# Optimization experiments

Measured on AMD Instinct MI355X. Metric: run time of the kernel, lower is better.

Reference implementation:

```python
import jax, jax.numpy as jnp
import numpy as np

EPS = 0.05      # entropic regularization, matches eps arg in forward
ITERS = 100     # Sinkhorn fixed-point iterations (auction analog; converged math)

def setup_inputs() -> dict:
    key = jax.random.key(0)
    k1, k2 = jax.random.split(key)
    B, N, D = 16, 2048, 3
    x = jax.random.uniform(k1, (B, N, D), dtype=jnp.float32)
    y = jax.random.uniform(k2, (B, N, D), dtype=jnp.float32)
    return {"x": x, "y": y}

def _emd_mean(x, y):
    # pairwise squared distances: [B, N, N]
    x2 = jnp.sum(x * x, axis=-1)                      # [B, N]
    y2 = jnp.sum(y * y, axis=-1)                      # [B, N]
    xy = jnp.einsum('bnd,bmd->bnm', x, y)             # [B, N, N]
    C = x2[:, :, None] + y2[:, None, :] - 2.0 * xy
    C = jnp.maximum(C, 0.0)

    B, N, _ = C.shape
    logK = -C / EPS                                   # [B, N, N]
    log_mu = jnp.full((B, N), -jnp.log(jnp.float32(N)))
    log_nu = log_mu

    def body(carry, _):
        f, g = carry
        # f_i = eps*(log mu_i - logsumexp_j((g_j - C_ij)/eps))
        f = EPS * (log_mu - jax.nn.logsumexp(logK + (g / EPS)[:, None, :], axis=2))
        g = EPS * (log_nu - jax.nn.logsumexp(logK + (f / EPS)[:, :, None], axis=1))
        return (f, g), None

    f0 = jnp.zeros((B, N), dtype=C.dtype)
    g0 = jnp.zeros((B, N), dtype=C.dtype)
    (f, g), _ = jax.lax.scan(body, (f0, g0), None, length=ITERS)

    # transport plan P_ij = exp((f_i + g_j - C_ij)/eps) (already includes mu,nu)
    logP = (f[:, :, None] + g[:, None, :] - C) / EPS
    P = jnp.exp(logP)
    # per-source-point matched squared distance, scaled by N (row mass = 1/N)
    dis = jnp.sum(P * C, axis=2) * N                  # [B, N]
    return dis.mean()

def reference(x, y):
    return _emd_mean(x, y)
```

## Files before the change

### kernel.cpp

```cpp
#include <hip/hip_runtime.h>

#define BB 16
#define NN 2048
#define NITERS 100

#define K2E      28.853900817779268f
#define TWO_K2E  57.707801635558536f
#define INV2K    0.017328679513998632f
#define INV_K2E  0.034657359027997264f
#define INV4K    0.008664339756999316f
#define LMU      (-11.0f)

#if __has_builtin(__builtin_amdgcn_exp2f)
#define EXP2F(x) __builtin_amdgcn_exp2f(x)
#else
#define EXP2F(x) exp2f(x)
#endif

typedef float v2f __attribute__((ext_vector_type(2)));
typedef float v4f __attribute__((ext_vector_type(4)));

#define DSTORE(p, v) __hip_atomic_store((p), (v), __ATOMIC_RELAXED, __HIP_MEMORY_SCOPE_AGENT)
#define DLOAD(p)     __hip_atomic_load((p), __ATOMIC_RELAXED, __HIP_MEMORY_SCOPE_AGENT)

__device__ __forceinline__ float bfly8(const float acc[8], int lane) {
    const bool b0 = lane & 1, b1 = lane & 2, b2 = lane & 4;
    float v4[4], v2_[2], v1;
    #pragma unroll
    for (int i = 0; i < 4; ++i) {
        float recv = __shfl_xor(b0 ? acc[i] : acc[i+4], 1, 64);
        v4[i] = (b0 ? acc[i+4] : acc[i]) + recv;
    }
    #pragma unroll
    for (int i = 0; i < 2; ++i) {
        float recv = __shfl_xor(b1 ? v4[i] : v4[i+2], 2, 64);
        v2_[i] = (b1 ? v4[i+2] : v4[i]) + recv;
    }
    {
        float recv = __shfl_xor(b2 ? v2_[0] : v2_[1], 4, 64);
        v1 = (b2 ? v2_[1] : v2_[0]) + recv;
    }
    v1 += __shfl_xor(v1, 8, 64);
    v1 += __shfl_xor(v1, 16, 64);
    v1 += __shfl_xor(v1, 32, 64);
    return v1;
}

__device__ __forceinline__ float sumpassF(
    const v4f* __restrict__ U, const v4f* __restrict__ T,
    const float* __restrict__ sdv,
    int rloc, int lane)
{
    v2f xp0[4], xp1[4], xp2[4], acc2[4];
    #pragma unroll
    for (int p = 0; p < 4; ++p) {
        const v4f ua = U[rloc + 2*p];
        const v4f ub = U[rloc + 2*p + 1];
        xp0[p] = (v2f){ua.x * INV2K, ub.x * INV2K};
        xp1[p] = (v2f){ua.y * INV2K, ub.y * INV2K};
        xp2[p] = (v2f){ua.z * INV2K, ub.z * INV2K};
        acc2[p] = (v2f){0.f, 0.f};
    }
    #pragma unroll 4
    for (int s = 0; s < 32; ++s) {
        const int p = lane + (s << 6);
        const v4f t = T[p];
        const float ad = sdv[p];
        const v2f a0v = (v2f){t.x, t.x}, a1v = (v2f){t.y, t.y};
        const v2f a2v = (v2f){t.z, t.z}, adv = (v2f){ad, ad};
        #pragma unroll
        for (int qq = 0; qq < 4; ++qq) {
            v2f d = __builtin_elementwise_fma(xp0[qq], a0v,
                    __builtin_elementwise_fma(xp1[qq], a1v,
                    __builtin_elementwise_fma(xp2[qq], a2v, adv)));
            acc2[qq] += (v2f){EXP2F(d.x), EXP2F(d.y)};
        }
    }
    float acc[8];
    #pragma unroll
    for (int p = 0; p < 4; ++p) { acc[2*p] = acc2[p].x; acc[2*p+1] = acc2[p].y; }
    return bfly8(acc, lane);
}

__device__ __forceinline__ float sumpassL(
    const v4f* __restrict__ U, const v4f* __restrict__ T,
    const float* __restrict__ sdv,
    int rloc, int jh, int lane, int w, float* pcomb)
{
    const int jb = (jh << 10) + lane;
    float dv[16];
    #pragma unroll
    for (int s = 0; s < 16; ++s)
        dv[s] = sdv[jb + (s << 6)];

    v2f xp0[4], xp1[4], xp2[4], acc2[4];
    #pragma unroll
    for (int p = 0; p < 4; ++p) {
        const v4f ua = U[rloc + 2*p];
        const v4f ub = U[rloc + 2*p + 1];
        xp0[p] = (v2f){ua.x * INV2K, ub.x * INV2K};
        xp1[p] = (v2f){ua.y * INV2K, ub.y * INV2K};
        xp2[p] = (v2f){ua.z * INV2K, ub.z * INV2K};
        acc2[p] = (v2f){0.f, 0.f};
    }
    #pragma unroll 4
    for (int s = 0; s < 16; ++s) {
        const v4f t = T[jb + (s << 6)];
        const float ad = dv[s];
        const v2f a0v = (v2f){t.x, t.x}, a1v = (v2f){t.y, t.y};
        const v2f a2v = (v2f){t.z, t.z}, adv = (v2f){ad, ad};
        #pragma unroll
        for (int qq = 0; qq < 4; ++qq) {
            v2f d = __builtin_elementwise_fma(xp0[qq], a0v,
                    __builtin_elementwise_fma(xp1[qq], a1v,
                    __builtin_elementwise_fma(xp2[qq], a2v, adv)));
            acc2[qq] += (v2f){EXP2F(d.x), EXP2F(d.y)};
        }
    }
    float acc[8];
    #pragma unroll
    for (int p = 0; p < 4; ++p) { acc[2*p] = acc2[p].x; acc[2*p+1] = acc2[p].y; }
    float v1 = bfly8(acc, lane);
    const int rr = ((lane & 1) << 2) | (lane & 2) | ((lane >> 2) & 1);
    if (lane < 8) pcomb[w * 8 + rr] = v1;
    __syncthreads();
    float Sc = 0.f;
    if (lane < 8) Sc = v1 + pcomb[(w ^ 1) * 8 + rr];
    return Sc;
}

__device__ __forceinline__ float epilA(
    const v4f* __restrict__ U, const v4f* __restrict__ T,
    const float* __restrict__ gB,
    float Aval, int rloc, int jh, int lane)
{
    const int jb = (jh << 10) + lane;
    float dv[16];
    #pragma unroll
    for (int s = 0; s < 16; ++s)
        dv[s] = DLOAD(gB + jb + (s << 6));

    float xr0[8], xr1[8], xr2[8], Ak[8], x2k[8];
    #pragma unroll
    for (int k = 0; k < 8; ++k) {
        const v4f u = U[rloc + k];
        xr0[k] = u.x * INV2K;
        xr1[k] = u.y * INV2K;
        xr2[k] = u.z * INV2K;
        const int src = ((k & 1) << 2) | (k & 2) | ((k >> 2) & 1);
        Ak[k]  = __shfl(Aval, src, 64);
        x2k[k] = K2E * (xr0[k]*xr0[k] + xr1[k]*xr1[k] + xr2[k]*xr2[k]);
    }
    float acc = 0.f;
    for (int s = 0; s < 16; ++s) {
        const v4f t = T[jb + (s << 6)];
        const float a0 = t.x, a1 = t.y, a2 = t.z, tb = dv[s];
        const float q2 = (a0*a0 + a1*a1 + a2*a2) * INV4K;
        #pragma unroll
        for (int k = 0; k < 8; ++k) {
            float d = fmaf(xr0[k], a0, fmaf(xr1[k], a1, fmaf(xr2[k], a2, tb)));
            float P = EXP2F(d + Ak[k]);
            float C = fmaxf((x2k[k] + q2 - (d - tb)) * INV_K2E, 0.f);
            acc = fmaf(P, C, acc);
        }
    }
    return acc;
}

__global__ __launch_bounds__(1024, 4) void emd_sinkhornU(
    const float* __restrict__ x, const float* __restrict__ y,
    float* __restrict__ Af, float* __restrict__ Bf,
    int* __restrict__ flags, float* __restrict__ out)
{
    extern __shared__ float S[];
    __shared__ float wsum[16];

    const int tid  = threadIdx.x;
    const int lane = tid & 63;
    const int w    = tid >> 6;
    const int blk  = blockIdx.x;
    const int b    = blk >> 4;
    const int q    = blk & 15;
    const int base = b * NN;
    const int row0 = q * 128;
    const int rloc = row0 + w * 8;
    int* fb = flags + b * 64;

    v4f   *sy = (v4f*)S;
    v4f   *sx = (v4f*)S + NN;
    float *sd = (float*)((v4f*)S + 2 * NN);

    #pragma unroll
    for (int v = 0; v < 2; ++v) {
        const int p = tid + (v << 10);
        const float* px = x + 3 * (size_t)(base + p);
        sx[p] = (v4f){TWO_K2E * px[0], TWO_K2E * px[1], TWO_K2E * px[2], 0.f};
        const float* py = y + 3 * (size_t)(base + p);
        sy[p] = (v4f){TWO_K2E * py[0], TWO_K2E * py[1], TWO_K2E * py[2], 0.f};
    }
    if (tid < 128) {
        const int col = row0 + tid;
        const float* py = y + 3 * (size_t)(base + col);
        const float a = py[0], bb = py[1], c = py[2];
        DSTORE(&Bf[base + col], -K2E * (a*a + bb*bb + c*c));
    }
    __syncthreads();
    if (tid == 0)
        __hip_atomic_store(fb + q * 4, 1, __ATOMIC_RELEASE, __HIP_MEMORY_SCOPE_AGENT);

    #define WAITB(tgt) do { __syncthreads();                                    \
        if (w == 0) {                                                           \
            for (;;) {                                                          \
                int vv = (lane < 16)                                            \
                    ? __hip_atomic_load(fb + lane * 4, __ATOMIC_RELAXED,        \
                                        __HIP_MEMORY_SCOPE_AGENT)               \
                    : 0x7fffffff;                                               \
                if (__ballot(vv >= (tgt)) == ~0ULL) break;                      \
                __builtin_amdgcn_s_sleep(1);                                    \
            }                                                                   \
        }                                                                       \
        __syncthreads(); } while (0)

    #define POSTB(pval) do { __syncthreads();                                   \
        if (tid == 0)                                                           \
            __hip_atomic_store(fb + q * 4, (pval), __ATOMIC_RELEASE,            \
                               __HIP_MEMORY_SCOPE_AGENT);                       \
    } while (0)

    #define STAGE(gsrc) do {                                                    \
        float t0_ = DLOAD((gsrc) + tid);                                        \
        float t1_ = DLOAD((gsrc) + tid + 1024);                                 \
        sd[tid] = t0_; sd[tid + 1024] = t1_;                                    \
        __syncthreads(); } while (0)

    WAITB(1);

    const int rr = ((lane & 1) << 2) | (lane & 2) | ((lane >> 2) & 1);
    float Aval = 0.f;

    for (int it = 0; it < NITERS; ++it) {
        STAGE(Bf + base);
        {
            float v1 = sumpassF(sx, sy, sd, rloc, lane);
            Aval = LMU - __log2f(v1);
            if (lane < 8) DSTORE(&Af[base + rloc + rr], Aval);
        }
        POSTB(2 * it + 2);
        WAITB(2 * it + 2);
        STAGE(Af + base);
        {
            float v1 = sumpassF(sy, sx, sd, rloc, lane);
            if (lane < 8)
                DSTORE(&Bf[base + rloc + rr], LMU - __log2f(v1));
        }
        POSTB(2 * it + 3);
        WAITB(2 * it + 3);
    }

    {
        float s = epilA(sx, sy, Bf + base, Aval, rloc, 0, lane)
                + epilA(sx, sy, Bf + base, Aval, rloc, 1, lane);
        #pragma unroll
        for (int m = 32; m > 0; m >>= 1) s += __shfl_xor(s, m, 64);
        if (lane == 0) wsum[w] = s;
        __syncthreads();
        if (tid == 0) {
            float t = 0.f;
            #pragma unroll
            for (int i = 0; i < 16; ++i) t += wsum[i];
            atomicAdd(out, t * (1.0f / (float)BB));
        }
    }
    #undef WAITB
    #undef POSTB
    #undef STAGE
}

__global__ __launch_bounds__(1024, 4) void emd_sinkhornT(
    const float* __restrict__ x, const float* __restrict__ y,
    float* __restrict__ Af, float* __restrict__ Bf,
    int* __restrict__ flags, float* __restrict__ out)
{
    extern __shared__ float S[];
    __shared__ float pcomb[16 * 8];
    __shared__ float wsum[16];

    const int tid  = threadIdx.x;
    const int lane = tid & 63;
    const int w    = tid >> 6;
    const int pr   = w >> 1;
    const int jh   = w & 1;
    const int blk  = blockIdx.x;
    const int b    = blk >> 4;
    const int q    = blk & 15;
    const int base = b * NN;
    const int row0 = q * 128;
    const int rlocA = row0 + pr * 8;
    const int rlocB = row0 + 64 + pr * 8;
    int* fb = flags + b * 64;

    v4f   *sy = (v4f*)S;
    v4f   *sx = (v4f*)S + NN;
    float *sd = (float*)((v4f*)S + 2 * NN);

    #pragma unroll
    for (int v = 0; v < 2; ++v) {
        const int p = tid + (v << 10);
        const float* px = x + 3 * (size_t)(base + p);
        sx[p] = (v4f){TWO_K2E * px[0], TWO_K2E * px[1], TWO_K2E * px[2], 0.f};
        const float* py = y + 3 * (size_t)(base + p);
        sy[p] = (v4f){TWO_K2E * py[0], TWO_K2E * py[1], TWO_K2E * py[2], 0.f};
    }
    if (tid < 128) {
        const int col = row0 + tid;
        const float* py = y + 3 * (size_t)(base + col);
        const float a = py[0], bb = py[1], c = py[2];
        DSTORE(&Bf[base + col], -K2E * (a*a + bb*bb + c*c));
    }
    __syncthreads();
    if (tid == 0)
        __hip_atomic_store(fb + q * 4, 1, __ATOMIC_RELEASE, __HIP_MEMORY_SCOPE_AGENT);

    #define WAITB2(tgt) do { __syncthreads();                                   \
        if (w == 0) {                                                           \
            for (;;) {                                                          \
                int vv = (lane < 16)                                            \
                    ? __hip_atomic_load(fb + lane * 4, __ATOMIC_RELAXED,        \
                                        __HIP_MEMORY_SCOPE_AGENT)               \
                    : 0x7fffffff;                                               \
                if (__ballot(vv >= (tgt)) == ~0ULL) break;                      \
                __builtin_amdgcn_s_sleep(1);                                    \
            }                                                                   \
        }                                                                       \
        __syncthreads(); } while (0)

    #define POSTB2(pval) do { __syncthreads();                                  \
        if (tid == 0)                                                           \
            __hip_atomic_store(fb + q * 4, (pval), __ATOMIC_RELEASE,            \
                               __HIP_MEMORY_SCOPE_AGENT);                       \
    } while (0)

    #define STAGE2(gsrc) do {                                                   \
        float t0_ = DLOAD((gsrc) + tid);                                        \
        float t1_ = DLOAD((gsrc) + tid + 1024);                                 \
        sd[tid] = t0_; sd[tid + 1024] = t1_;                                    \
        __syncthreads(); } while (0)

    WAITB2(1);

    const int rr = ((lane & 1) << 2) | (lane & 2) | ((lane >> 2) & 1);
    float Aval0 = 0.f, Aval1 = 0.f;

    for (int it = 0; it < NITERS; ++it) {
        STAGE2(Bf + base);
        {
            float Sc = sumpassL(sx, sy, sd, rlocA, jh, lane, w, pcomb);
            Aval0 = LMU - __log2f(Sc);
            if (lane < 8 && jh == 0) DSTORE(&Af[base + rlocA + rr], Aval0);
        }
        {
            float Sc = sumpassL(sx, sy, sd, rlocB, jh, lane, w, pcomb);
            Aval1 = LMU - __log2f(Sc);
            if (lane < 8 && jh == 0) DSTORE(&Af[base + rlocB + rr], Aval1);
        }
        POSTB2(2 * it + 2);
        WAITB2(2 * it + 2);
        STAGE2(Af + base);
        {
            float Sc = sumpassL(sy, sx, sd, rlocA, jh, lane, w, pcomb);
            if (lane < 8 && jh == 0)
                DSTORE(&Bf[base + rlocA + rr], LMU - __log2f(Sc));
        }
        {
            float Sc = sumpassL(sy, sx, sd, rlocB, jh, lane, w, pcomb);
            if (lane < 8 && jh == 0)
                DSTORE(&Bf[base + rlocB + rr], LMU - __log2f(Sc));
        }
        POSTB2(2 * it + 3);
        WAITB2(2 * it + 3);
    }

    {
        float s = epilA(sx, sy, Bf + base, Aval0, rlocA, jh, lane)
                + epilA(sx, sy, Bf + base, Aval1, rlocB, jh, lane);
        #pragma unroll
        for (int m = 32; m > 0; m >>= 1) s += __shfl_xor(s, m, 64);
        if (lane == 0) wsum[w] = s;
        __syncthreads();
        if (tid == 0) {
            float t = 0.f;
            #pragma unroll
            for (int i = 0; i < 16; ++i) t += wsum[i];
            atomicAdd(out, t * (1.0f / (float)BB));
        }
    }
    #undef WAITB2
    #undef POSTB2
    #undef STAGE2
}

extern "C" void kernel_launch(void* const* d_in, const int* in_sizes, int n_in,
                              void* d_out, int out_size, void* d_ws, size_t ws_size,
                              hipStream_t stream) {
    const float* x = (const float*)d_in[0];
    const float* y = (const float*)d_in[1];
    float* out = (float*)d_out;
    char* ws = (char*)d_ws;

    int*   flags = (int*)ws;
    float* Af    = (float*)(ws + 16384);
    float* Bf    = (float*)(ws + 16384 + (size_t)BB*NN*sizeof(float));

    hipMemsetAsync(flags, 0, 16384, stream);
    hipMemsetAsync(out, 0, sizeof(float), stream);

    void* args[] = {(void*)&x, (void*)&y, (void*)&Af, (void*)&Bf,
                    (void*)&flags, (void*)&out};

    const size_t shmem = (size_t)(2 * NN * 4 + NN) * sizeof(float);
    hipError_t eu = hipFuncSetAttribute((const void*)emd_sinkhornU,
                        hipFuncAttributeMaxDynamicSharedMemorySize, (int)shmem);
    hipError_t e = (eu == hipSuccess)
        ? hipLaunchCooperativeKernel((const void*)emd_sinkhornU,
                                     dim3(256), dim3(1024), args, shmem, stream)
        : hipErrorInvalidValue;
    if (e != hipSuccess) {
        hipError_t et = hipFuncSetAttribute((const void*)emd_sinkhornT,
                            hipFuncAttributeMaxDynamicSharedMemorySize, (int)shmem);
        hipError_t e2 = (et == hipSuccess)
            ? hipLaunchCooperativeKernel((const void*)emd_sinkhornT,
                                         dim3(256), dim3(1024), args, shmem, stream)
            : hipErrorInvalidValue;
        if (e2 != hipSuccess) {
            hipLaunchKernelGGL(emd_sinkhornT, dim3(256), dim3(1024), shmem,
                               stream, x, y, Af, Bf, flags, out);
        }
    }
}
```

Measured before the change: 2.337 ms.

## Split work across 512 blocks of 512 threads per batch

Adds a new primary kernel that splits each batch across 32 blocks of 64 rows and 512 threads instead of 16 blocks of 128 rows and 1024 threads, with a 32-slot flag barrier. The old 1024-thread kernel becomes the fallback, and the split-row kernel is removed. The intent is to fill more CUs (512 blocks versus 256 on the device) so that more of the exp2 throughput is used. In exchange, each barrier has twice as many participants and each block stages the full x, y and dual vectors into shared memory, doubling redundant staging traffic.

Measured after the change: 2.496 ms. 6.8% more time.

```diff
diff --git a/kernel.cpp b/kernel.cpp
--- a/kernel.cpp
+++ b/kernel.cpp
@@ -82,53 +82,6 @@
     return bfly8(acc, lane);
 }
 
-__device__ __forceinline__ float sumpassL(
-    const v4f* __restrict__ U, const v4f* __restrict__ T,
-    const float* __restrict__ sdv,
-    int rloc, int jh, int lane, int w, float* pcomb)
-{
-    const int jb = (jh << 10) + lane;
-    float dv[16];
-    #pragma unroll
-    for (int s = 0; s < 16; ++s)
-        dv[s] = sdv[jb + (s << 6)];
-
-    v2f xp0[4], xp1[4], xp2[4], acc2[4];
-    #pragma unroll
-    for (int p = 0; p < 4; ++p) {
-        const v4f ua = U[rloc + 2*p];
-        const v4f ub = U[rloc + 2*p + 1];
-        xp0[p] = (v2f){ua.x * INV2K, ub.x * INV2K};
-        xp1[p] = (v2f){ua.y * INV2K, ub.y * INV2K};
-        xp2[p] = (v2f){ua.z * INV2K, ub.z * INV2K};
-        acc2[p] = (v2f){0.f, 0.f};
-    }
-    #pragma unroll 4
-    for (int s = 0; s < 16; ++s) {
-        const v4f t = T[jb + (s << 6)];
-        const float ad = dv[s];
-        const v2f a0v = (v2f){t.x, t.x}, a1v = (v2f){t.y, t.y};
-        const v2f a2v = (v2f){t.z, t.z}, adv = (v2f){ad, ad};
-        #pragma unroll
-        for (int qq = 0; qq < 4; ++qq) {
-            v2f d = __builtin_elementwise_fma(xp0[qq], a0v,
-                    __builtin_elementwise_fma(xp1[qq], a1v,
-                    __builtin_elementwise_fma(xp2[qq], a2v, adv)));
-            acc2[qq] += (v2f){EXP2F(d.x), EXP2F(d.y)};
-        }
-    }
-    float acc[8];
-    #pragma unroll
-    for (int p = 0; p < 4; ++p) { acc[2*p] = acc2[p].x; acc[2*p+1] = acc2[p].y; }
-    float v1 = bfly8(acc, lane);
-    const int rr = ((lane & 1) << 2) | (lane & 2) | ((lane >> 2) & 1);
-    if (lane < 8) pcomb[w * 8 + rr] = v1;
-    __syncthreads();
-    float Sc = 0.f;
-    if (lane < 8) Sc = v1 + pcomb[(w ^ 1) * 8 + rr];
-    return Sc;
-}
-
 __device__ __forceinline__ float epilA(
     const v4f* __restrict__ U, const v4f* __restrict__ T,
     const float* __restrict__ gB,
@@ -167,6 +120,118 @@
     return acc;
 }
 
+__global__ __launch_bounds__(512, 4) void emd_sinkhornV(
+    const float* __restrict__ x, const float* __restrict__ y,
+    float* __restrict__ Af, float* __restrict__ Bf,
+    int* __restrict__ flags, float* __restrict__ out)
+{
+    extern __shared__ float S[];
+    __shared__ float wsum[8];
+
+    const int tid  = threadIdx.x;
+    const int lane = tid & 63;
+    const int w    = tid >> 6;
+    const int blk  = blockIdx.x;
+    const int b    = blk >> 5;
+    const int q    = blk & 31;
+    const int base = b * NN;
+    const int row0 = q * 64;
+    const int rloc = row0 + w * 8;
+    int* fb = flags + b * 128;
+
+    v4f   *sy = (v4f*)S;
+    v4f   *sx = (v4f*)S + NN;
+    float *sd = (float*)((v4f*)S + 2 * NN);
+
+    #pragma unroll
+    for (int v = 0; v < 4; ++v) {
+        const int p = tid + (v << 9);
+        const float* px = x + 3 * (size_t)(base + p);
+        sx[p] = (v4f){TWO_K2E * px[0], TWO_K2E * px[1], TWO_K2E * px[2], 0.f};
+        const float* py = y + 3 * (size_t)(base + p);
+        sy[p] = (v4f){TWO_K2E * py[0], TWO_K2E * py[1], TWO_K2E * py[2], 0.f};
+    }
+    if (tid < 64) {
+        const int col = row0 + tid;
+        const float* py = y + 3 * (size_t)(base + col);
+        const float a = py[0], bb = py[1], c = py[2];
+        DSTORE(&Bf[base + col], -K2E * (a*a + bb*bb + c*c));
+    }
+    __syncthreads();
+    if (tid == 0)
+        __hip_atomic_store(fb + q * 4, 1, __ATOMIC_RELEASE, __HIP_MEMORY_SCOPE_AGENT);
+
+    #define WAITB(tgt) do { __syncthreads();                                    \
+        if (w == 0) {                                                           \
+            for (;;) {                                                          \
+                int vv = (lane < 32)                                            \
+                    ? __hip_atomic_load(fb + lane * 4, __ATOMIC_RELAXED,        \
+                                        __HIP_MEMORY_SCOPE_AGENT)               \
+                    : 0x7fffffff;                                               \
+                if (__ballot(vv >= (tgt)) == ~0ULL) break;                      \
+                __builtin_amdgcn_s_sleep(1);                                    \
+            }                                                                   \
+        }                                                                       \
+        __syncthreads(); } while (0)
+
+    #define POSTB(pval) do { __syncthreads();                                   \
+        if (tid == 0)                                                           \
+            __hip_atomic_store(fb + q * 4, (pval), __ATOMIC_RELEASE,            \
+                               __HIP_MEMORY_SCOPE_AGENT);                       \
+    } while (0)
+
+    #define STAGE(gsrc) do {                                                    \
+        float t0_ = DLOAD((gsrc) + tid);                                        \
+        float t1_ = DLOAD((gsrc) + tid + 512);                                  \
+        float t2_ = DLOAD((gsrc) + tid + 1024);                                 \
+        float t3_ = DLOAD((gsrc) + tid + 1536);                                 \
+        sd[tid] = t0_; sd[tid + 512] = t1_;                                     \
+        sd[tid + 1024] = t2_; sd[tid + 1536] = t3_;                             \
+        __syncthreads(); } while (0)
+
+    WAITB(1);
+
+    const int rr = ((lane & 1) << 2) | (lane & 2) | ((lane >> 2) & 1);
+    float Aval = 0.f;
+
+    for (int it = 0; it < NITERS; ++it) {
+        STAGE(Bf + base);
+        {
+            float v1 = sumpassF(sx, sy, sd, rloc, lane);
+            Aval = LMU - __log2f(v1);
+            if (lane < 8) DSTORE(&Af[base + rloc + rr], Aval);
+        }
+        POSTB(2 * it + 2);
+        WAITB(2 * it + 2);
+        STAGE(Af + base);
+        {
+            float v1 = sumpassF(sy, sx, sd, rloc, lane);
+            if (lane < 8)
+                DSTORE(&Bf[base + rloc + rr], LMU - __log2f(v1));
+        }
+        POSTB(2 * it + 3);
+        WAITB(2 * it + 3);
+    }
+
+    {
+        float s = epilA(sx, sy, Bf + base, Aval, rloc, 0, lane)
+                + epilA(sx, sy, Bf + base, Aval, rloc, 1, lane);
+        #pragma unroll
+        for (int m = 32; m > 0; m >>= 1) s += __shfl_xor(s, m, 64);
+        if (lane == 0) wsum[w] = s;
+        __syncthreads();
+        if (tid == 0) {
+            float t = 0.f;
+            #pragma unroll
+            for (int i = 0; i < 8; ++i) t += wsum[i];
+            atomicAdd(out, t * (1.0f / (float)BB));
+        }
+    }
+    #undef WAITB
+    #undef POSTB
+    #undef STAGE
+}
+
 __global__ __launch_bounds__(1024, 4) void emd_sinkhornU(
     const float* __restrict__ x, const float* __restrict__ y,
     float* __restrict__ Af, float* __restrict__ Bf,
@@ -184,7 +249,7 @@
     const int base = b * NN;
     const int row0 = q * 128;
     const int rloc = row0 + w * 8;
-    int* fb = flags + b * 64;
+    int* fb = flags + 2048 + b * 64;
 
     v4f   *sy = (v4f*)S;
     v4f   *sx = (v4f*)S + NN;
@@ -208,7 +273,7 @@
     if (tid == 0)
         __hip_atomic_store(fb + q * 4, 1, __ATOMIC_RELEASE, __HIP_MEMORY_SCOPE_AGENT);
 
-    #define WAITB(tgt) do { __syncthreads();                                    \
+    #define WAITB2(tgt) do { __syncthreads();                                   \
         if (w == 0) {                                                           \
             for (;;) {                                                          \
                 int vv = (lane < 16)                                            \
@@ -221,40 +286,40 @@
         }                                                                       \
         __syncthreads(); } while (0)
 
-    #define POSTB(pval) do { __syncthreads();                                   \
+    #define POSTB2(pval) do { __syncthreads();                                  \
         if (tid == 0)                                                           \
             __hip_atomic_store(fb + q * 4, (pval), __ATOMIC_RELEASE,            \
                                __HIP_MEMORY_SCOPE_AGENT);                       \
     } while (0)
 
-    #define STAGE(gsrc) do {                                                    \
+    #define STAGE2(gsrc) do {                                                   \
         float t0_ = DLOAD((gsrc) + tid);                                        \
         float t1_ = DLOAD((gsrc) + tid + 1024);                                 \
         sd[tid] = t0_; sd[tid + 1024] = t1_;                                    \
         __syncthreads(); } while (0)
 
-    WAITB(1);
+    WAITB2(1);
 
     const int rr = ((lane & 1) << 2) | (lane & 2) | ((lane >> 2) & 1);
     float Aval = 0.f;
 
     for (int it = 0; it < NITERS; ++it) {
-        STAGE(Bf + base);
+        STAGE2(Bf + base);
         {
             float v1 = sumpassF(sx, sy, sd, rloc, lane);
             Aval = LMU - __log2f(v1);
             if (lane < 8) DSTORE(&Af[base + rloc + rr], Aval);
         }
-        POSTB(2 * it + 2);
-        WAITB(2 * it + 2);
-        STAGE(Af + base);
+        POSTB2(2 * it + 2);
+        WAITB2(2 * it + 2);
+        STAGE2(Af + base);
         {
             float v1 = sumpassF(sy, sx, sd, rloc, lane);
             if (lane < 8)
                 DSTORE(&Bf[base + rloc + rr], LMU - __log2f(v1));
         }
-        POSTB(2 * it + 3);
-        WAITB(2 * it + 3);
+        POSTB2(2 * it + 3);
+        WAITB2(2 * it + 3);
     }
 
     {
@@ -271,129 +336,6 @@
             atomicAdd(out, t * (1.0f / (float)BB));
         }
     }
-    #undef WAITB
-    #undef POSTB
-    #undef STAGE
-}
-
-__global__ __launch_bounds__(1024, 4) void emd_sinkhornT(
-    const float* __restrict__ x, const float* __restrict__ y,
-    float* __restrict__ Af, float* __restrict__ Bf,
-    int* __restrict__ flags, float* __restrict__ out)
-{
-    extern __shared__ float S[];
-    __shared__ float pcomb[16 * 8];
-    __shared__ float wsum[16];
-
-    const int tid  = threadIdx.x;
-    const int lane = tid & 63;
-    const int w    = tid >> 6;
-    const int pr   = w >> 1;
-    const int jh   = w & 1;
-    const int blk  = blockIdx.x;
-    const int b    = blk >> 4;
-    const int q    = blk & 15;
-    const int base = b * NN;
-    const int row0 = q * 128;
-    const int rlocA = row0 + pr * 8;
-    const int rlocB = row0 + 64 + pr * 8;
-    int* fb = flags + b * 64;
-
-    v4f   *sy = (v4f*)S;
-    v4f   *sx = (v4f*)S + NN;
-    float *sd = (float*)((v4f*)S + 2 * NN);
-
-    #pragma unroll
-    for (int v = 0; v < 2; ++v) {
-        const int p = tid + (v << 10);
-        const float* px = x + 3 * (size_t)(base + p);
-        sx[p] = (v4f){TWO_K2E * px[0], TWO_K2E * px[1], TWO_K2E * px[2], 0.f};
-        const float* py = y + 3 * (size_t)(base + p);
-        sy[p] = (v4f){TWO_K2E * py[0], TWO_K2E * py[1], TWO_K2E * py[2], 0.f};
-    }
-    if (tid < 128) {
-        const int col = row0 + tid;
-        const float* py = y + 3 * (size_t)(base + col);
-        const float a = py[0], bb = py[1], c = py[2];
-        DSTORE(&Bf[base + col], -K2E * (a*a + bb*bb + c*c));
-    }
-    __syncthreads();
-    if (tid == 0)
-        __hip_atomic_store(fb + q * 4, 1, __ATOMIC_RELEASE, __HIP_MEMORY_SCOPE_AGENT);
-
-    #define WAITB2(tgt) do { __syncthreads();                                   \
-        if (w == 0) {                                                           \
-            for (;;) {                                                          \
-                int vv = (lane < 16)                                            \
-                    ? __hip_atomic_load(fb + lane * 4, __ATOMIC_RELAXED,        \
-                                        __HIP_MEMORY_SCOPE_AGENT)               \
-                    : 0x7fffffff;                                               \
-                if (__ballot(vv >= (tgt)) == ~0ULL) break;                      \
-                __builtin_amdgcn_s_sleep(1);                                    \
-            }                                                                   \
-        }                                                                       \
-        __syncthreads(); } while (0)
-
-    #define POSTB2(pval) do { __syncthreads();                                  \
-        if (tid == 0)                                                           \
-            __hip_atomic_store(fb + q * 4, (pval), __ATOMIC_RELEASE,            \
-                               __HIP_MEMORY_SCOPE_AGENT);                       \
-    } while (0)
-
-    #define STAGE2(gsrc) do {                                                   \
-        float t0_ = DLOAD((gsrc) + tid);                                        \
-        float t1_ = DLOAD((gsrc) + tid + 1024);                                 \
-        sd[tid] = t0_; sd[tid + 1024] = t1_;                                    \
-        __syncthreads(); } while (0)
-
-    WAITB2(1);
-
-    const int rr = ((lane & 1) << 2) | (lane & 2) | ((lane >> 2) & 1);
-    float Aval0 = 0.f, Aval1 = 0.f;
-
-    for (int it = 0; it < NITERS; ++it) {
-        STAGE2(Bf + base);
-        {
-            float Sc = sumpassL(sx, sy, sd, rlocA, jh, lane, w, pcomb);
-            Aval0 = LMU - __log2f(Sc);
-            if (lane < 8 && jh == 0) DSTORE(&Af[base + rlocA + rr], Aval0);
-        }
-        {
-            float Sc = sumpassL(sx, sy, sd, rlocB, jh, lane, w, pcomb);
-            Aval1 = LMU - __log2f(Sc);
-            if (lane < 8 && jh == 0) DSTORE(&Af[base + rlocB + rr], Aval1);
-        }
-        POSTB2(2 * it + 2);
-        WAITB2(2 * it + 2);
-        STAGE2(Af + base);
-        {
-            float Sc = sumpassL(sy, sx, sd, rlocA, jh, lane, w, pcomb);
-            if (lane < 8 && jh == 0)
-                DSTORE(&Bf[base + rlocA + rr], LMU - __log2f(Sc));
-        }
-        {
-            float Sc = sumpassL(sy, sx, sd, rlocB, jh, lane, w, pcomb);
-            if (lane < 8 && jh == 0)
-                DSTORE(&Bf[base + rlocB + rr], LMU - __log2f(Sc));
-        }
-        POSTB2(2 * it + 3);
-        WAITB2(2 * it + 3);
-    }
-
-    {
-        float s = epilA(sx, sy, Bf + base, Aval0, rlocA, jh, lane)
-                + epilA(sx, sy, Bf + base, Aval1, rlocB, jh, lane);
-        #pragma unroll
-        for (int m = 32; m > 0; m >>= 1) s += __shfl_xor(s, m, 64);
-        if (lane == 0) wsum[w] = s;
-        __syncthreads();
-        if (tid == 0) {
-            float t = 0.f;
-            #pragma unroll
-            for (int i = 0; i < 16; ++i) t += wsum[i];
-            atomicAdd(out, t * (1.0f / (float)BB));
-        }
-    }
     #undef WAITB2
     #undef POSTB2
     #undef STAGE2
@@ -418,21 +360,21 @@
                     (void*)&flags, (void*)&out};
 
     const size_t shmem = (size_t)(2 * NN * 4 + NN) * sizeof(float);
-    hipError_t eu = hipFuncSetAttribute((const void*)emd_sinkhornU,
+    hipError_t ev = hipFuncSetAttribute((const void*)emd_sinkhornV,
                         hipFuncAttributeMaxDynamicSharedMemorySize, (int)shmem);
-    hipError_t e = (eu == hipSuccess)
-        ? hipLaunchCooperativeKernel((const void*)emd_sinkhornU,
-                                     dim3(256), dim3(1024), args, shmem, stream)
+    hipError_t e = (ev == hipSuccess)
+        ? hipLaunchCooperativeKernel((const void*)emd_sinkhornV,
+                                     dim3(512), dim3(512), args, shmem, stream)
         : hipErrorInvalidValue;
     if (e != hipSuccess) {
-        hipError_t et = hipFuncSetAttribute((const void*)emd_sinkhornT,
+        hipError_t eu = hipFuncSetAttribute((const void*)emd_sinkhornU,
                             hipFuncAttributeMaxDynamicSharedMemorySize, (int)shmem);
-        hipError_t e2 = (et == hipSuccess)
-            ? hipLaunchCooperativeKernel((const void*)emd_sinkhornT,
+        hipError_t e2 = (eu == hipSuccess)
+            ? hipLaunchCooperativeKernel((const void*)emd_sinkhornU,
                                          dim3(256), dim3(1024), args, shmem, stream)
             : hipErrorInvalidValue;
         if (e2 != hipSuccess) {
-            hipLaunchKernelGGL(emd_sinkhornT, dim3(256), dim3(1024), shmem,
+            hipLaunchKernelGGL(emd_sinkhornU, dim3(256), dim3(1024), shmem,
                                stream, x, y, Af, Bf, flags, out);
         }
     }
```
